# Performance work log

Measured on AMD Instinct MI355X. Metric: run time of the kernel, lower is better.

## Reference

```python
import jax, jax.numpy as jnp
import numpy as np

SHAPELET_SIZE = 64
NUM_SHAPELETS = 128
IN_CHANNELS = 8


def setup_inputs() -> dict:
    key = jax.random.key(0)
    k1, k2 = jax.random.split(key)
    x = jax.random.normal(k1, (64, IN_CHANNELS, 2048), dtype=jnp.float32)
    shapelets = jax.random.normal(k2, (IN_CHANNELS, NUM_SHAPELETS, SHAPELET_SIZE), dtype=jnp.float32)
    return {"x": x, "shapelets": shapelets}


def _znorm(s):
    # Z-normalize along the time-step axis (dim 2), matching Znormalize_dim(shapelets, 2)
    mu = jnp.mean(s, axis=2, keepdims=True)
    sd = jnp.std(s, axis=2, keepdims=True)
    return (s - mu) / sd


def reference(x, shapelets):
    # x: (N, C, L); shapelets: (C, K, S)
    S = shapelets.shape[-1]
    N, C, L = x.shape
    W = L - S + 1
    # unfold(2, S, 1): sliding windows -> (N, C, W, S)
    idx = jnp.arange(W)[:, None] + jnp.arange(S)[None, :]  # (W, S)
    xw = x[:, :, idx]  # (N, C, W, S)
    sh = _znorm(shapelets)  # (C, K, S)
    # Euclidean cdist via ||a||^2 + ||b||^2 - 2 a.b (avoids (N,C,W,K,S) blowup)
    sq_x = jnp.sum(xw * xw, axis=-1)          # (N, C, W)
    sq_s = jnp.sum(sh * sh, axis=-1)          # (C, K)
    cross = jnp.einsum('ncws,cks->ncwk', xw, sh)  # (N, C, W, K)
    d2 = sq_x[..., None] + sq_s[None, :, None, :] - 2.0 * cross
    d = jnp.sqrt(jnp.maximum(d2, 1e-12))      # (N, C, W, K)
    # sum over channels, then global min over windows -> (N, 1, K)
    dsum = jnp.sum(d, axis=1)                 # (N, W, K)
    out = jnp.min(dsum, axis=1)[:, None, :]   # (N, 1, K)
    return out
```

## Files before the change

kernel.cpp:

```cpp
#include <hip/hip_runtime.h>
#include <hip/hip_bf16.h>
#include <math.h>

#define C 8
#define K 128
#define S 64
#define L 2048
#define NB 64
#define W (L - S + 1)
#define TW 128
#define NTW 16
#define XCS 208
#define XFS 200

typedef __attribute__((ext_vector_type(8))) short bf16x8;
typedef __attribute__((ext_vector_type(4))) float f32x4;

__device__ __forceinline__ unsigned short f2bf(float f) {
  unsigned int u = __float_as_uint(f);
  u += 0x7FFFu + ((u >> 16) & 1u);
  return (unsigned short)(u >> 16);
}

__device__ __forceinline__ unsigned int pkbf(float a, float b) {
  __hip_bfloat162 h = __float22bfloat162_rn(make_float2(a, b));
  return *reinterpret_cast<unsigned int*>(&h);
}

__global__ __launch_bounds__(256) void prep_kernel(const float* __restrict__ sh,
                                                   unsigned short* __restrict__ shzB,
                                                   float* __restrict__ out) {
  int tid = blockIdx.x * 256 + threadIdx.x;
  if (tid < NB * K) out[tid] = __int_as_float(0x7F800000);
  int gid = blockIdx.x * 4 + (threadIdx.x >> 6);
  int lane = threadIdx.x & 63;
  float v = sh[(size_t)gid * S + lane];
  float s1 = v, s2 = v * v;
#pragma unroll
  for (int off = 32; off > 0; off >>= 1) {
    s1 += __shfl_down(s1, off);
    s2 += __shfl_down(s2, off);
  }
  s1 = __shfl(s1, 0);
  s2 = __shfl(s2, 0);
  float mu = s1 * (1.0f / S);
  float sd = sqrtf(fmaxf(s2 * (1.0f / S) - mu * mu, 0.0f));
  float z = (v - mu) / sd;
  int c = gid >> 7, k = gid & (K - 1), s = lane;
  int idx = c * 8192 + (k >> 6) * 4096 + ((((k >> 4) & 3) * 2) + (s >> 5)) * 512 +
            ((((s >> 3) & 3) * 16 + (k & 15)) * 8) + (s & 7);
  shzB[idx] = f2bf(-2.0f * z);
}

#define WT_COMPUTE(WT, P)                                                     \
  {                                                                           \
    bf16x8 x0 = *(const bf16x8*)(xc + abase + (WT) * 16);                     \
    bf16x8 x1 = *(const bf16x8*)(xc + abase + (WT) * 16 + 32);                \
    f32x4 ai = *(const f32x4*)&sqx[c][wgrp * 64 + (WT) * 16 + quad * 4];      \
    P[0] = __builtin_amdgcn_mfma_f32_16x16x32_bf16(x0, Bc[0], ai, 0, 0, 0);   \
    P[1] = __builtin_amdgcn_mfma_f32_16x16x32_bf16(x0, Bc[2], ai, 0, 0, 0);   \
    P[2] = __builtin_amdgcn_mfma_f32_16x16x32_bf16(x0, Bc[4], ai, 0, 0, 0);   \
    P[3] = __builtin_amdgcn_mfma_f32_16x16x32_bf16(x0, Bc[6], ai, 0, 0, 0);   \
    P[0] = __builtin_amdgcn_mfma_f32_16x16x32_bf16(x1, Bc[1], P[0], 0, 0, 0); \
    P[1] = __builtin_amdgcn_mfma_f32_16x16x32_bf16(x1, Bc[3], P[1], 0, 0, 0); \
    P[2] = __builtin_amdgcn_mfma_f32_16x16x32_bf16(x1, Bc[5], P[2], 0, 0, 0); \
    P[3] = __builtin_amdgcn_mfma_f32_16x16x32_bf16(x1, Bc[7], P[3], 0, 0, 0); \
  }

#define WT_SQRT(WT, P)                                                        \
  {                                                                           \
    _Pragma("unroll")                                                         \
    for (int i = 0; i < 4; ++i) {                                             \
      dsum[0][WT][i] += __builtin_amdgcn_sqrtf(__builtin_fabsf(P[0][i]));     \
      dsum[1][WT][i] += __builtin_amdgcn_sqrtf(__builtin_fabsf(P[1][i]));     \
      dsum[2][WT][i] += __builtin_amdgcn_sqrtf(__builtin_fabsf(P[2][i]));     \
      dsum[3][WT][i] += __builtin_amdgcn_sqrtf(__builtin_fabsf(P[3][i]));     \
    }                                                                         \
  }

__global__ __launch_bounds__(256, 3) void main_kernel(const float* __restrict__ x,
                                                      const unsigned short* __restrict__ shzB,
                                                      int* __restrict__ out) {
  __shared__ __align__(16) unsigned short xcop[C][8][XCS];
  __shared__ __align__(16) float sqx[C][TW];
  __shared__ __align__(16) float xf[C][XFS];

  const int t = threadIdx.x;
  const int lane = t & 63;
  const int wave = t >> 6;
  const int wgrp = wave & 1;
  const int kgrp = wave >> 1;
  const int col = lane & 15;
  const int quad = lane >> 4;
  const int n = blockIdx.y;
  const int w0 = blockIdx.x * TW;
  const float* xn = x + (size_t)n * C * L;
  const unsigned short* bw = shzB + kgrp * 4096 + lane * 8;
  const int cbase = (2 * wave + blockIdx.x + blockIdx.y) & 7;

  float* xfp = &xf[0][0];
#pragma unroll
  for (int cc = 0; cc < 2; ++cc) {
    const int c = wave * 2 + cc;
    const int e = lane * 4;
    float4 v; v.x = v.y = v.z = v.w = 0.0f;
    if (lane < 48) {
      int g = w0 + e;
      if (g + 3 < L) {
        v = *(const float4*)(xn + c * L + g);
      } else {
        v.x = (g + 0 < L) ? xn[c * L + g + 0] : 0.0f;
        v.y = (g + 1 < L) ? xn[c * L + g + 1] : 0.0f;
        v.z = (g + 2 < L) ? xn[c * L + g + 2] : 0.0f;
        v.w = (g + 3 < L) ? xn[c * L + g + 3] : 0.0f;
      }
    }
    if (lane < 50) *(float4*)&xfp[c * XFS + e] = v;
  }
  __syncthreads();

#pragma unroll
  for (int cc = 0; cc < 2; ++cc) {
    const int cb = wave * 2 + cc;
    const int rb = lane >> 3;
    const int c8 = lane & 7;
    const float* xr = xfp + cb * XFS;
#pragma unroll
    for (int j = 0; j < 12; ++j) {
      int i = (c8 + j * 8) * 2;
      *(unsigned int*)&xcop[cb][rb][i] = pkbf(xr[i + rb], xr[i + rb + 1]);
    }
  }
#pragma unroll
  for (int cc = 0; cc < 2; ++cc) {
    const int c = wave * 2 + cc, wl = lane * 2;
    const float* xr = xfp + c * XFS;
    float p0 = 0.f, p1 = 0.f, p2 = 0.f, p3 = 0.f;
#pragma unroll
    for (int si = 0; si < S; si += 4) {
      float v0 = xr[wl + si], v1 = xr[wl + si + 1], v2 = xr[wl + si + 2], v3 = xr[wl + si + 3];
      p0 = fmaf(v0, v0, p0); p1 = fmaf(v1, v1, p1);
      p2 = fmaf(v2, v2, p2); p3 = fmaf(v3, v3, p3);
    }
    float s0 = 64.0f + (p0 + p1) + (p2 + p3);
    sqx[c][wl] = s0;
    float a = xr[wl + S], b = xr[wl];
    sqx[c][wl + 1] = s0 + a * a - b * b;
  }
  __syncthreads();

  const f32x4 z4 = {0.0f, 0.0f, 0.0f, 0.0f};
  f32x4 dsum[4][4];
#pragma unroll
  for (int kt = 0; kt < 4; ++kt)
#pragma unroll
    for (int wt = 0; wt < 4; ++wt) dsum[kt][wt] = z4;

  const int r8 = col & 7;
  const int abase = wgrp * 64 + (col - r8) + quad * 8;

  for (int ci = 0; ci < C; ++ci) {
    const int c = (cbase + ci) & 7;

    bf16x8 Bc[8];
#pragma unroll
    for (int i = 0; i < 8; ++i)
      Bc[i] = *(const bf16x8*)(bw + c * 8192 + i * 512);

    const unsigned short* xc = &xcop[c][r8][0];

    f32x4 pA[4], pB[4];
    WT_COMPUTE(0, pA)
    WT_COMPUTE(1, pB)
    WT_SQRT(0, pA)
    WT_COMPUTE(2, pA)
    WT_SQRT(1, pB)
    WT_COMPUTE(3, pB)
    WT_SQRT(2, pA)
    WT_SQRT(3, pB)
  }

  const float INF = __int_as_float(0x7F800000);
  const int wbase = w0 + wgrp * 64;
#pragma unroll
  for (int kt = 0; kt < 4; ++kt) {
    float mv = INF;
#pragma unroll
    for (int wt = 0; wt < 4; ++wt)
#pragma unroll
      for (int i = 0; i < 4; ++i) {
        int w = wbase + wt * 16 + quad * 4 + i;
        mv = (w < W) ? fminf(mv, dsum[kt][wt][i]) : mv;
      }
    mv = fminf(mv, __shfl_xor(mv, 16));
    mv = fminf(mv, __shfl_xor(mv, 32));
    if (quad == 0)
      atomicMin(&out[n * K + kgrp * 64 + kt * 16 + col], __float_as_int(mv));
  }
}

extern "C" void kernel_launch(void* const* d_in, const int* in_sizes, int n_in,
                              void* d_out, int out_size, void* d_ws, size_t ws_size,
                              hipStream_t stream) {
  const float* x = (const float*)d_in[0];
  const float* sh = (const float*)d_in[1];
  float* out = (float*)d_out;
  unsigned short* shzB = (unsigned short*)d_ws;

  prep_kernel<<<256, 256, 0, stream>>>(sh, shzB, out);
  main_kernel<<<dim3(NTW, NB), 256, 0, stream>>>(x, shzB, (int*)out);
}
```

Baseline: 82.27 us.

## Halve window tile and split shapelets across four waves per block

Shrinks the window tile from 128 to 64 and doubles the grid, so each of the four waves now covers 32 shapelets over all 64 windows instead of 64 shapelets over half the windows. Per-wave accumulators and B-fragment registers are halved, and the occupancy hint rises from 3 to 4 blocks per SIMD. The aim is more parallelism and better latency hiding. In exchange, the x staging, bf16 conversion and per-window squared-norm work are repeated for twice as many blocks, and the block halo overhead grows relative to useful work.

```diff
diff --git a/kernel.cpp b/kernel.cpp
--- a/kernel.cpp
+++ b/kernel.cpp
@@ -8,10 +8,10 @@
 #define L 2048
 #define NB 64
 #define W (L - S + 1)
-#define TW 128
-#define NTW 16
-#define XCS 208
-#define XFS 200
+#define TW 64
+#define NTW 32
+#define XCS 144
+#define XFS 136
 
 typedef __attribute__((ext_vector_type(8))) short bf16x8;
 typedef __attribute__((ext_vector_type(4))) float f32x4;
@@ -56,15 +56,11 @@
   {                                                                           \
     bf16x8 x0 = *(const bf16x8*)(xc + abase + (WT) * 16);                     \
     bf16x8 x1 = *(const bf16x8*)(xc + abase + (WT) * 16 + 32);                \
-    f32x4 ai = *(const f32x4*)&sqx[c][wgrp * 64 + (WT) * 16 + quad * 4];      \
+    f32x4 ai = *(const f32x4*)&sqx[c][(WT) * 16 + quad * 4];                  \
     P[0] = __builtin_amdgcn_mfma_f32_16x16x32_bf16(x0, Bc[0], ai, 0, 0, 0);   \
     P[1] = __builtin_amdgcn_mfma_f32_16x16x32_bf16(x0, Bc[2], ai, 0, 0, 0);   \
-    P[2] = __builtin_amdgcn_mfma_f32_16x16x32_bf16(x0, Bc[4], ai, 0, 0, 0);   \
-    P[3] = __builtin_amdgcn_mfma_f32_16x16x32_bf16(x0, Bc[6], ai, 0, 0, 0);   \
     P[0] = __builtin_amdgcn_mfma_f32_16x16x32_bf16(x1, Bc[1], P[0], 0, 0, 0); \
     P[1] = __builtin_amdgcn_mfma_f32_16x16x32_bf16(x1, Bc[3], P[1], 0, 0, 0); \
-    P[2] = __builtin_amdgcn_mfma_f32_16x16x32_bf16(x1, Bc[5], P[2], 0, 0, 0); \
-    P[3] = __builtin_amdgcn_mfma_f32_16x16x32_bf16(x1, Bc[7], P[3], 0, 0, 0); \
   }
 
 #define WT_SQRT(WT, P)                                                        \
@@ -73,12 +69,10 @@
     for (int i = 0; i < 4; ++i) {                                             \
       dsum[0][WT][i] += __builtin_amdgcn_sqrtf(__builtin_fabsf(P[0][i]));     \
       dsum[1][WT][i] += __builtin_amdgcn_sqrtf(__builtin_fabsf(P[1][i]));     \
-      dsum[2][WT][i] += __builtin_amdgcn_sqrtf(__builtin_fabsf(P[2][i]));     \
-      dsum[3][WT][i] += __builtin_amdgcn_sqrtf(__builtin_fabsf(P[3][i]));     \
     }                                                                         \
   }
 
-__global__ __launch_bounds__(256, 3) void main_kernel(const float* __restrict__ x,
+__global__ __launch_bounds__(256, 4) void main_kernel(const float* __restrict__ x,
                                                       const unsigned short* __restrict__ shzB,
                                                       int* __restrict__ out) {
   __shared__ __align__(16) unsigned short xcop[C][8][XCS];
@@ -88,14 +82,14 @@
   const int t = threadIdx.x;
   const int lane = t & 63;
   const int wave = t >> 6;
-  const int wgrp = wave & 1;
-  const int kgrp = wave >> 1;
+  const int kgrp = wave;
   const int col = lane & 15;
   const int quad = lane >> 4;
   const int n = blockIdx.y;
   const int w0 = blockIdx.x * TW;
   const float* xn = x + (size_t)n * C * L;
-  const unsigned short* bw = shzB + kgrp * 4096 + lane * 8;
+  const unsigned short* bw =
+      shzB + ((kgrp >> 1) * 8 + (kgrp & 1) * 4) * 512 + lane * 8;
   const int cbase = (2 * wave + blockIdx.x + blockIdx.y) & 7;
 
   float* xfp = &xf[0][0];
@@ -104,7 +98,7 @@
     const int c = wave * 2 + cc;
     const int e = lane * 4;
     float4 v; v.x = v.y = v.z = v.w = 0.0f;
-    if (lane < 48) {
+    if (lane < 32) {
       int g = w0 + e;
       if (g + 3 < L) {
         v = *(const float4*)(xn + c * L + g);
@@ -115,7 +109,7 @@
         v.w = (g + 3 < L) ? xn[c * L + g + 3] : 0.0f;
       }
     }
-    if (lane < 50) *(float4*)&xfp[c * XFS + e] = v;
+    if (lane < 34) *(float4*)&xfp[c * XFS + e] = v;
   }
   __syncthreads();
 
@@ -126,50 +120,47 @@
     const int c8 = lane & 7;
     const float* xr = xfp + cb * XFS;
 #pragma unroll
-    for (int j = 0; j < 12; ++j) {
+    for (int j = 0; j < 8; ++j) {
       int i = (c8 + j * 8) * 2;
       *(unsigned int*)&xcop[cb][rb][i] = pkbf(xr[i + rb], xr[i + rb + 1]);
     }
   }
 #pragma unroll
   for (int cc = 0; cc < 2; ++cc) {
-    const int c = wave * 2 + cc, wl = lane * 2;
-    const float* xr = xfp + c * XFS;
+    const int c = wave * 2 + cc;
+    const float* xr = xfp + c * XFS + lane;
     float p0 = 0.f, p1 = 0.f, p2 = 0.f, p3 = 0.f;
 #pragma unroll
     for (int si = 0; si < S; si += 4) {
-      float v0 = xr[wl + si], v1 = xr[wl + si + 1], v2 = xr[wl + si + 2], v3 = xr[wl + si + 3];
+      float v0 = xr[si], v1 = xr[si + 1], v2 = xr[si + 2], v3 = xr[si + 3];
       p0 = fmaf(v0, v0, p0); p1 = fmaf(v1, v1, p1);
       p2 = fmaf(v2, v2, p2); p3 = fmaf(v3, v3, p3);
     }
-    float s0 = 64.0f + (p0 + p1) + (p2 + p3);
-    sqx[c][wl] = s0;
-    float a = xr[wl + S], b = xr[wl];
-    sqx[c][wl + 1] = s0 + a * a - b * b;
+    sqx[c][lane] = 64.0f + (p0 + p1) + (p2 + p3);
   }
   __syncthreads();
 
   const f32x4 z4 = {0.0f, 0.0f, 0.0f, 0.0f};
-  f32x4 dsum[4][4];
-#pragma unroll
-  for (int kt = 0; kt < 4; ++kt)
+  f32x4 dsum[2][4];
+#pragma unroll
+  for (int kt = 0; kt < 2; ++kt)
 #pragma unroll
     for (int wt = 0; wt < 4; ++wt) dsum[kt][wt] = z4;
 
   const int r8 = col & 7;
-  const int abase = wgrp * 64 + (col - r8) + quad * 8;
+  const int abase = (col - r8) + quad * 8;
 
   for (int ci = 0; ci < C; ++ci) {
     const int c = (cbase + ci) & 7;
 
-    bf16x8 Bc[8];
-#pragma unroll
-    for (int i = 0; i < 8; ++i)
+    bf16x8 Bc[4];
+#pragma unroll
+    for (int i = 0; i < 4; ++i)
       Bc[i] = *(const bf16x8*)(bw + c * 8192 + i * 512);
 
     const unsigned short* xc = &xcop[c][r8][0];
 
-    f32x4 pA[4], pB[4];
+    f32x4 pA[2], pB[2];
     WT_COMPUTE(0, pA)
     WT_COMPUTE(1, pB)
     WT_SQRT(0, pA)
@@ -181,21 +172,20 @@
   }
 
   const float INF = __int_as_float(0x7F800000);
-  const int wbase = w0 + wgrp * 64;
-#pragma unroll
-  for (int kt = 0; kt < 4; ++kt) {
+#pragma unroll
+  for (int kt = 0; kt < 2; ++kt) {
     float mv = INF;
 #pragma unroll
     for (int wt = 0; wt < 4; ++wt)
 #pragma unroll
       for (int i = 0; i < 4; ++i) {
-        int w = wbase + wt * 16 + quad * 4 + i;
+        int w = w0 + wt * 16 + quad * 4 + i;
         mv = (w < W) ? fminf(mv, dsum[kt][wt][i]) : mv;
       }
     mv = fminf(mv, __shfl_xor(mv, 16));
     mv = fminf(mv, __shfl_xor(mv, 32));
     if (quad == 0)
-      atomicMin(&out[n * K + kgrp * 64 + kt * 16 + col], __float_as_int(mv));
+      atomicMin(&out[n * K + kgrp * 32 + kt * 16 + col], __float_as_int(mv));
   }
 }
 
```

Result: slower. 109.8 us (+33.4%).
